# Performance work log

Hardware: AMD Instinct MI355X
Metric: run time of the kernel (lower is better)

Reference implementation:

```python
import jax, jax.numpy as jnp
import numpy as np

N = 50000   # nodes
E = 800000  # edges (avg degree 16)
D = 128     # hidden_channels
L = 4       # num_layers
ALPHA = 0.1


def setup_inputs() -> dict:
    key = jax.random.key(0)
    ks = jax.random.split(key, 6)
    x = jax.random.normal(ks[0], (N, D), dtype=jnp.float32)
    w = jax.random.uniform(ks[1], (E,), dtype=jnp.float32)
    src = jax.random.randint(ks[2], (E,), 0, N)
    dst = jax.random.randint(ks[3], (E,), 0, N)
    # stacked per-layer Linear params
    W = jax.random.normal(ks[4], (L, D, D), dtype=jnp.float32) / np.float32(np.sqrt(D))
    b = jax.random.normal(ks[5], (L, D), dtype=jnp.float32) * 0.01
    # GPR coefficients: alpha*(1-alpha)^k, last = (1-alpha)^L
    temp_np = ALPHA * (1 - ALPHA) ** np.arange(L + 1)
    temp_np[-1] = (1 - ALPHA) ** L
    temp = jnp.asarray(temp_np, dtype=jnp.float32)
    return {"x": x, "w": w, "src": src, "dst": dst, "W": W, "b": b, "temp": temp}


def reference(x, w, src, dst, W, b, temp):
    # eval mode: dropout / dropout_adj are no-ops; edge_attn=False
    hidden = x * temp[0]
    for i in range(L):
        h = x @ W[i] + b[i]                 # [N, D] linear
        msg = h[src] * w[:, None]           # gather + edge-weight, [E, D]
        x = jax.ops.segment_sum(msg, dst, num_segments=N)  # scatter-sum
        x = jax.nn.relu(x)
        hidden = hidden + x * temp[i + 1]
    return hidden
```

## Files before the change

kernel.cpp:

```cpp
#include <hip/hip_runtime.h>
#include <hip/hip_fp16.h>

#define N_NODES 50000
#define N_EDGES 800000
#define DIM 128
#define LAYERS 4
#define SLOT 48
#define EPB 8
#define CNT_STRIDE 6250

#define BUCKET_BLOCKS 3128
#define WT_BLOCKS 256
#define INIT_BLOCKS 3125

typedef __attribute__((ext_vector_type(8))) _Float16 half8;
typedef __attribute__((ext_vector_type(4))) float float4v;
typedef __attribute__((ext_vector_type(2))) float float2v;

__device__ __forceinline__ int pack_edge(int s, float w) {
    return (int)(((unsigned)__half_as_ushort(__float2half(w)) << 16) | (unsigned)(s & 0xFFFF));
}

__device__ __forceinline__ void fp8x8_to_f32(uint2 v, float* f) {
    float2v a = __builtin_amdgcn_cvt_pk_f32_fp8(v.x, false);
    float2v b = __builtin_amdgcn_cvt_pk_f32_fp8(v.x, true);
    float2v c = __builtin_amdgcn_cvt_pk_f32_fp8(v.y, false);
    float2v d = __builtin_amdgcn_cvt_pk_f32_fp8(v.y, true);
    f[0] = a[0]; f[1] = a[1]; f[2] = b[0]; f[3] = b[1];
    f[4] = c[0]; f[5] = c[1]; f[6] = d[0]; f[7] = d[1];
}

__device__ __forceinline__ uint2 f32x8_to_fp8(const float* f) {
    unsigned lo = 0, hi = 0;
    lo = __builtin_amdgcn_cvt_pk_fp8_f32(f[0], f[1], lo, false);
    lo = __builtin_amdgcn_cvt_pk_fp8_f32(f[2], f[3], lo, true);
    hi = __builtin_amdgcn_cvt_pk_fp8_f32(f[4], f[5], hi, false);
    hi = __builtin_amdgcn_cvt_pk_fp8_f32(f[6], f[7], hi, true);
    return make_uint2(lo, hi);
}

__device__ __forceinline__ void bucket_one(int d, int s, float wv, int g,
                                           int* __restrict__ cnt,
                                           int* __restrict__ edge_buf) {
    if ((d & 7) == g) {
        int pos = atomicAdd(&cnt[g * CNT_STRIDE + (d >> 3)], 1);
        edge_buf[(size_t)d * SLOT + pos] = pack_edge(s, wv);
    }
}

__global__ __launch_bounds__(256) void prep_kernel(const int* __restrict__ src,
                                                   const int* __restrict__ dst,
                                                   const float* __restrict__ w,
                                                   int* __restrict__ cnt,
                                                   int* __restrict__ edge_buf,
                                                   const float* __restrict__ W,
                                                   __half* __restrict__ Wt,
                                                   const float4* __restrict__ x,
                                                   uint2* __restrict__ xh0) {
    int bid = blockIdx.x;
    int tid = threadIdx.x;
    if (bid < BUCKET_BLOCKS) {
        int g     = bid & 7;
        int chunk = bid >> 3;
        int base  = (chunk * 256 + tid) * EPB;
        if (base >= N_EDGES) return;
        int4   d4a = *(const int4*)(dst + base);
        int4   d4b = *(const int4*)(dst + base + 4);
        int4   s4a = *(const int4*)(src + base);
        int4   s4b = *(const int4*)(src + base + 4);
        float4 w4a = *(const float4*)(w + base);
        float4 w4b = *(const float4*)(w + base + 4);
        bucket_one(d4a.x, s4a.x, w4a.x, g, cnt, edge_buf);
        bucket_one(d4a.y, s4a.y, w4a.y, g, cnt, edge_buf);
        bucket_one(d4a.z, s4a.z, w4a.z, g, cnt, edge_buf);
        bucket_one(d4a.w, s4a.w, w4a.w, g, cnt, edge_buf);
        bucket_one(d4b.x, s4b.x, w4b.x, g, cnt, edge_buf);
        bucket_one(d4b.y, s4b.y, w4b.y, g, cnt, edge_buf);
        bucket_one(d4b.z, s4b.z, w4b.z, g, cnt, edge_buf);
        bucket_one(d4b.w, s4b.w, w4b.w, g, cnt, edge_buf);
    } else if (bid < BUCKET_BLOCKS + WT_BLOCKS) {
        int i = (bid - BUCKET_BLOCKS) * 256 + tid;
        int l   = i >> 14;
        int rem = i & 16383;
        int k = rem >> 7;
        int n = rem & 127;
        Wt[(size_t)l * DIM * DIM + n * DIM + k] =
            __float2half(W[(size_t)l * DIM * DIM + k * DIM + n]);
    } else {
        int i = (bid - BUCKET_BLOCKS - WT_BLOCKS) * 256 + tid;
        float4 a = x[(size_t)i * 2];
        float4 b = x[(size_t)i * 2 + 1];
        float f[8] = { a.x, a.y, a.z, a.w, b.x, b.y, b.z, b.w };
        xh0[i] = f32x8_to_fp8(f);
    }
}

__device__ __forceinline__ void batch8(const uint2* __restrict__ x8,
                                       int m, int base, int cnt_r, int r, int c,
                                       float* accf, float& wsum) {
    uint2 v[8]; float wv[8];
    #pragma unroll
    for (int u = 0; u < 8; ++u) {
        int jj = base + u;
        int p  = __shfl(m, (r << 4) | (jj & 15), 64);
        bool live = (jj < cnt_r);
        wv[u] = live
                  ? __half2float(__ushort_as_half((unsigned short)((unsigned)p >> 16)))
                  : 0.f;
        uint2 vv = make_uint2(0u, 0u);
        if (live) vv = x8[(size_t)(p & 0xFFFF) * 16 + c];
        v[u] = vv;
    }
    #pragma unroll
    for (int u = 0; u < 8; ++u) {
        wsum += wv[u];
        float f[8];
        fp8x8_to_f32(v[u], f);
        #pragma unroll
        for (int t = 0; t < 8; ++t)
            accf[t] += wv[u] * f[t];
    }
}

#define AP 136
template <bool FINAL>
__global__ __launch_bounds__(256) void layer_kernel(const uint2* __restrict__ xin8,
                                                    const int* __restrict__ cnt_arr,
                                                    const int* __restrict__ edge_buf,
                                                    const __half* __restrict__ Wt,
                                                    const float* __restrict__ bl,
                                                    uint2* __restrict__ xout,
                                                    float* __restrict__ hidden,
                                                    const float* __restrict__ temp,
                                                    const uint2* __restrict__ x0h,
                                                    const uint2* __restrict__ x1h,
                                                    const uint2* __restrict__ x2h) {
    __shared__ __half Ah[16][AP];
    __shared__ float winS[16];
    int tid  = threadIdx.x;
    int wave = tid >> 6;
    int lane = tid & 63;
    int r = lane >> 4;
    int c = lane & 15;
    int node0  = blockIdx.x * 16 + wave * 4;
    int node_r = node0 + r;

    size_t mb = (size_t)node_r * SLOT;
    int m0 = edge_buf[mb + c];
    int m1 = edge_buf[mb + 16 + c];
    int cnt_r = cnt_arr[(node_r & 7) * CNT_STRIDE + (node_r >> 3)];

    int maxc = cnt_r;
    maxc = max(maxc, __shfl_xor(maxc, 16, 64));
    maxc = max(maxc, __shfl_xor(maxc, 32, 64));

    float accf[8];
    #pragma unroll
    for (int t = 0; t < 8; ++t) accf[t] = 0.f;
    float wsum = 0.f;

    batch8(xin8, m0, 0, cnt_r, r, c, accf, wsum);
    batch8(xin8, m0, 8, cnt_r, r, c, accf, wsum);
    if (maxc > 16) {
        batch8(xin8, m1, 16, cnt_r, r, c, accf, wsum);
        batch8(xin8, m1, 24, cnt_r, r, c, accf, wsum);
    }
    if (maxc > 32) {
        int m2 = edge_buf[mb + 32 + c];
        batch8(xin8, m2, 32, cnt_r, r, c, accf, wsum);
        batch8(xin8, m2, 40, cnt_r, r, c, accf, wsum);
    }

    union { __half2 hh[4]; float4 f4; } ua;
    ua.hh[0] = __floats2half2_rn(accf[0], accf[1]);
    ua.hh[1] = __floats2half2_rn(accf[2], accf[3]);
    ua.hh[2] = __floats2half2_rn(accf[4], accf[5]);
    ua.hh[3] = __floats2half2_rn(accf[6], accf[7]);
    int lr = wave * 4 + r;
    *(float4*)&Ah[lr][c * 8] = ua.f4;
    if (c == 0) winS[lr] = wsum;
    __syncthreads();

    int am  = lane & 15;
    int ak8 = (lane >> 4) * 8;
    float4v acc0 = (float4v)(0.f), acc1 = (float4v)(0.f);
    #pragma unroll
    for (int kk = 0; kk < 4; ++kk) {
        int k0 = kk * 32 + ak8;
        half8 a  = *(const half8*)&Ah[am][k0];
        half8 b0 = *(const half8*)(Wt + (size_t)(wave * 32 + am) * DIM + k0);
        half8 b1 = *(const half8*)(Wt + (size_t)(wave * 32 + 16 + am) * DIM + k0);
        acc0 = __builtin_amdgcn_mfma_f32_16x16x32_f16(a, b0, acc0, 0, 0, 0);
        acc1 = __builtin_amdgcn_mfma_f32_16x16x32_f16(a, b1, acc1, 0, 0, 0);
    }
    __syncthreads();

    int q  = lane >> 4;
    int cc = lane & 15;
    {
        int col = wave * 32 + cc;
        float bv = bl[col];
        #pragma unroll
        for (int j = 0; j < 4; ++j) {
            int row = q * 4 + j;
            Ah[row][col] = __float2half(fmaxf(acc0[j] + winS[row] * bv, 0.f));
        }
        col = wave * 32 + 16 + cc;
        bv = bl[col];
        #pragma unroll
        for (int j = 0; j < 4; ++j) {
            int row = q * 4 + j;
            Ah[row][col] = __float2half(fmaxf(acc1[j] + winS[row] * bv, 0.f));
        }
    }
    __syncthreads();

    int row = tid >> 4;
    int ch  = tid & 15;
    int gnode = blockIdx.x * 16 + row;
    half8 hv = *(const half8*)&Ah[row][ch * 8];
    size_t ro = (size_t)gnode * 16 + ch;

    if constexpr (!FINAL) {
        float f[8];
        #pragma unroll
        for (int t = 0; t < 8; ++t) f[t] = (float)hv[t];
        xout[ro] = f32x8_to_fp8(f);
    } else {
        float t0 = temp[0], t1 = temp[1], t2 = temp[2], t3 = temp[3], t4 = temp[4];
        uint2 u0 = x0h[ro], u1 = x1h[ro], u2 = x2h[ro], u3 = xin8[ro];
        float f0[8], f1[8], f2[8], f3[8];
        fp8x8_to_f32(u0, f0);
        fp8x8_to_f32(u1, f1);
        fp8x8_to_f32(u2, f2);
        fp8x8_to_f32(u3, f3);
        float out[8];
        #pragma unroll
        for (int t = 0; t < 8; ++t)
            out[t] = t0 * f0[t] + t1 * f1[t] + t2 * f2[t]
                   + t3 * f3[t] + t4 * (float)hv[t];
        size_t o = (size_t)gnode * DIM + ch * 8;
        *(float4*)(hidden + o)     = make_float4(out[0], out[1], out[2], out[3]);
        *(float4*)(hidden + o + 4) = make_float4(out[4], out[5], out[6], out[7]);
    }
}

extern "C" void kernel_launch(void* const* d_in, const int* in_sizes, int n_in,
                              void* d_out, int out_size, void* d_ws, size_t ws_size,
                              hipStream_t stream) {
    const float* x    = (const float*)d_in[0];
    const float* w    = (const float*)d_in[1];
    const int*   src  = (const int*)d_in[2];
    const int*   dst  = (const int*)d_in[3];
    const float* W    = (const float*)d_in[4];
    const float* b    = (const float*)d_in[5];
    const float* temp = (const float*)d_in[6];
    float* hidden = (float*)d_out;

    char* ws = (char*)d_ws;
    uint2* X0 = (uint2*)ws;                  ws += (size_t)N_NODES * DIM;
    uint2* X1 = (uint2*)ws;                  ws += (size_t)N_NODES * DIM;
    uint2* X2 = (uint2*)ws;                  ws += (size_t)N_NODES * DIM;
    uint2* X3 = (uint2*)ws;                  ws += (size_t)N_NODES * DIM;
    __half* Wt = (__half*)ws;                ws += (size_t)LAYERS * DIM * DIM * sizeof(__half);
    int* cnt = (int*)ws;                     ws += (size_t)N_NODES * sizeof(int);
    int* edge_buf = (int*)ws;                ws += (size_t)(N_NODES * SLOT + 64) * sizeof(int);

    hipMemsetAsync(cnt, 0, (size_t)N_NODES * sizeof(int), stream);
    prep_kernel<<<BUCKET_BLOCKS + WT_BLOCKS + INIT_BLOCKS, 256, 0, stream>>>(
        src, dst, w, cnt, edge_buf, W, Wt, (const float4*)x, X0);

    const int layer_blocks = N_NODES / 16;
    layer_kernel<false><<<layer_blocks, 256, 0, stream>>>(
        X0, cnt, edge_buf, Wt + 0 * DIM * DIM, b + 0 * DIM,
        X1, hidden, temp, nullptr, nullptr, nullptr);
    layer_kernel<false><<<layer_blocks, 256, 0, stream>>>(
        X1, cnt, edge_buf, Wt + 1 * DIM * DIM, b + 1 * DIM,
        X2, hidden, temp, nullptr, nullptr, nullptr);
    layer_kernel<false><<<layer_blocks, 256, 0, stream>>>(
        X2, cnt, edge_buf, Wt + 2 * DIM * DIM, b + 2 * DIM,
        X3, hidden, temp, nullptr, nullptr, nullptr);
    layer_kernel<true><<<layer_blocks, 256, 0, stream>>>(
        X3, cnt, edge_buf, Wt + 3 * DIM * DIM, b + 3 * DIM,
        nullptr, hidden, temp, X0, X1, X2);
}
```

Baseline: 244.6 us.

## Process 32 nodes per block with 16-byte gathers and 8 lanes per node

Each layer block now handles 32 nodes instead of 16. Each node is served by 8 lanes that each gather 16 fp8 features (uint4) per edge, so every lane issues half as many wider loads. Each wave now computes a 16x64 tile of the 32x128 MFMA product, so each weight fragment is reused across more rows. The cost is twice the accumulator registers per lane, possible lower occupancy, and a bounds check for the last partial block.

```diff
diff --git a/kernel.cpp b/kernel.cpp
--- a/kernel.cpp
+++ b/kernel.cpp
@@ -12,6 +12,7 @@
 #define BUCKET_BLOCKS 3128
 #define WT_BLOCKS 256
 #define INIT_BLOCKS 3125
+#define LAYER_BLOCKS 1563
 
 typedef __attribute__((ext_vector_type(8))) _Float16 half8;
 typedef __attribute__((ext_vector_type(4))) float float4v;
@@ -95,36 +96,36 @@
     }
 }
 
-__device__ __forceinline__ void batch8(const uint2* __restrict__ x8,
-                                       int m, int base, int cnt_r, int r, int c,
-                                       float* accf, float& wsum) {
-    uint2 v[8]; float wv[8];
+__device__ __forceinline__ void batch8w(const uint4* __restrict__ x16,
+                                        int m, int base, int cnt_r, int sgb, int c2,
+                                        float* accf, float& wsum) {
+    uint4 v[8]; float wv[8];
     #pragma unroll
     for (int u = 0; u < 8; ++u) {
-        int jj = base + u;
-        int p  = __shfl(m, (r << 4) | (jj & 15), 64);
-        bool live = (jj < cnt_r);
+        int p = __shfl(m, sgb | u, 64);
+        bool live = (base + u) < cnt_r;
         wv[u] = live
                   ? __half2float(__ushort_as_half((unsigned short)((unsigned)p >> 16)))
                   : 0.f;
-        uint2 vv = make_uint2(0u, 0u);
-        if (live) vv = x8[(size_t)(p & 0xFFFF) * 16 + c];
+        uint4 vv = make_uint4(0u, 0u, 0u, 0u);
+        if (live) vv = x16[(size_t)(p & 0xFFFF) * 8 + c2];
         v[u] = vv;
     }
     #pragma unroll
     for (int u = 0; u < 8; ++u) {
         wsum += wv[u];
-        float f[8];
-        fp8x8_to_f32(v[u], f);
-        #pragma unroll
-        for (int t = 0; t < 8; ++t)
+        float f[16];
+        fp8x8_to_f32(make_uint2(v[u].x, v[u].y), f);
+        fp8x8_to_f32(make_uint2(v[u].z, v[u].w), f + 8);
+        #pragma unroll
+        for (int t = 0; t < 16; ++t)
             accf[t] += wv[u] * f[t];
     }
 }
 
 #define AP 136
 template <bool FINAL>
-__global__ __launch_bounds__(256) void layer_kernel(const uint2* __restrict__ xin8,
+__global__ __launch_bounds__(256) void layer_kernel(const uint4* __restrict__ xin16,
                                                     const int* __restrict__ cnt_arr,
                                                     const int* __restrict__ edge_buf,
                                                     const __half* __restrict__ Wt,
@@ -135,113 +136,126 @@
                                                     const uint2* __restrict__ x0h,
                                                     const uint2* __restrict__ x1h,
                                                     const uint2* __restrict__ x2h) {
-    __shared__ __half Ah[16][AP];
-    __shared__ float winS[16];
+    __shared__ __half Ah[32][AP];
+    __shared__ float winS[32];
     int tid  = threadIdx.x;
     int wave = tid >> 6;
     int lane = tid & 63;
-    int r = lane >> 4;
-    int c = lane & 15;
-    int node0  = blockIdx.x * 16 + wave * 4;
-    int node_r = node0 + r;
-
-    size_t mb = (size_t)node_r * SLOT;
-    int m0 = edge_buf[mb + c];
-    int m1 = edge_buf[mb + 16 + c];
-    int cnt_r = cnt_arr[(node_r & 7) * CNT_STRIDE + (node_r >> 3)];
+    int sg  = lane >> 3;
+    int c2  = lane & 7;
+    int sgb = lane & 0x38;
+    int node_r = blockIdx.x * 32 + wave * 8 + sg;
+    bool valid = node_r < N_NODES;
+    int nidx = valid ? node_r : 0;
+
+    size_t mb = (size_t)nidx * SLOT;
+    int m0 = edge_buf[mb + c2];
+    int m1 = edge_buf[mb + 8 + c2];
+    int m2 = edge_buf[mb + 16 + c2];
+    int m3 = edge_buf[mb + 24 + c2];
+    int cnt_r = valid ? cnt_arr[(nidx & 7) * CNT_STRIDE + (nidx >> 3)] : 0;
 
     int maxc = cnt_r;
+    maxc = max(maxc, __shfl_xor(maxc, 8, 64));
     maxc = max(maxc, __shfl_xor(maxc, 16, 64));
     maxc = max(maxc, __shfl_xor(maxc, 32, 64));
 
-    float accf[8];
-    #pragma unroll
-    for (int t = 0; t < 8; ++t) accf[t] = 0.f;
+    float accf[16];
+    #pragma unroll
+    for (int t = 0; t < 16; ++t) accf[t] = 0.f;
     float wsum = 0.f;
 
-    batch8(xin8, m0, 0, cnt_r, r, c, accf, wsum);
-    batch8(xin8, m0, 8, cnt_r, r, c, accf, wsum);
+    batch8w(xin16, m0, 0, cnt_r, sgb, c2, accf, wsum);
+    batch8w(xin16, m1, 8, cnt_r, sgb, c2, accf, wsum);
     if (maxc > 16) {
-        batch8(xin8, m1, 16, cnt_r, r, c, accf, wsum);
-        batch8(xin8, m1, 24, cnt_r, r, c, accf, wsum);
+        batch8w(xin16, m2, 16, cnt_r, sgb, c2, accf, wsum);
+        batch8w(xin16, m3, 24, cnt_r, sgb, c2, accf, wsum);
     }
     if (maxc > 32) {
-        int m2 = edge_buf[mb + 32 + c];
-        batch8(xin8, m2, 32, cnt_r, r, c, accf, wsum);
-        batch8(xin8, m2, 40, cnt_r, r, c, accf, wsum);
-    }
-
-    union { __half2 hh[4]; float4 f4; } ua;
-    ua.hh[0] = __floats2half2_rn(accf[0], accf[1]);
-    ua.hh[1] = __floats2half2_rn(accf[2], accf[3]);
-    ua.hh[2] = __floats2half2_rn(accf[4], accf[5]);
-    ua.hh[3] = __floats2half2_rn(accf[6], accf[7]);
-    int lr = wave * 4 + r;
-    *(float4*)&Ah[lr][c * 8] = ua.f4;
-    if (c == 0) winS[lr] = wsum;
+        int m4 = edge_buf[mb + 32 + c2];
+        int m5 = edge_buf[mb + 40 + c2];
+        batch8w(xin16, m4, 32, cnt_r, sgb, c2, accf, wsum);
+        batch8w(xin16, m5, 40, cnt_r, sgb, c2, accf, wsum);
+    }
+
+    {
+        union { __half2 hh[8]; float4 f4[2]; } ua;
+        #pragma unroll
+        for (int t = 0; t < 8; ++t)
+            ua.hh[t] = __floats2half2_rn(accf[2 * t], accf[2 * t + 1]);
+        int lr = wave * 8 + sg;
+        *(float4*)&Ah[lr][c2 * 16]     = ua.f4[0];
+        *(float4*)&Ah[lr][c2 * 16 + 8] = ua.f4[1];
+        if (c2 == 0) winS[lr] = wsum;
+    }
     __syncthreads();
 
     int am  = lane & 15;
     int ak8 = (lane >> 4) * 8;
-    float4v acc0 = (float4v)(0.f), acc1 = (float4v)(0.f);
+    int rt  = (wave & 1) * 16;
+    int ct  = (wave >> 1) * 64;
+    float4v acc[4];
+    #pragma unroll
+    for (int j = 0; j < 4; ++j) acc[j] = (float4v)(0.f);
     #pragma unroll
     for (int kk = 0; kk < 4; ++kk) {
         int k0 = kk * 32 + ak8;
-        half8 a  = *(const half8*)&Ah[am][k0];
-        half8 b0 = *(const half8*)(Wt + (size_t)(wave * 32 + am) * DIM + k0);
-        half8 b1 = *(const half8*)(Wt + (size_t)(wave * 32 + 16 + am) * DIM + k0);
-        acc0 = __builtin_amdgcn_mfma_f32_16x16x32_f16(a, b0, acc0, 0, 0, 0);
-        acc1 = __builtin_amdgcn_mfma_f32_16x16x32_f16(a, b1, acc1, 0, 0, 0);
+        half8 a = *(const half8*)&Ah[rt + am][k0];
+        #pragma unroll
+        for (int j = 0; j < 4; ++j) {
+            half8 bj = *(const half8*)(Wt + (size_t)(ct + j * 16 + am) * DIM + k0);
+            acc[j] = __builtin_amdgcn_mfma_f32_16x16x32_f16(a, bj, acc[j], 0, 0, 0);
+        }
     }
     __syncthreads();
 
-    int q  = lane >> 4;
-    int cc = lane & 15;
     {
-        int col = wave * 32 + cc;
-        float bv = bl[col];
+        int q  = lane >> 4;
+        int cc = lane & 15;
         #pragma unroll
         for (int j = 0; j < 4; ++j) {
-            int row = q * 4 + j;
-            Ah[row][col] = __float2half(fmaxf(acc0[j] + winS[row] * bv, 0.f));
+            int col = ct + j * 16 + cc;
+            float bv = bl[col];
+            #pragma unroll
+            for (int jj = 0; jj < 4; ++jj) {
+                int row = rt + q * 4 + jj;
+                Ah[row][col] = __float2half(fmaxf(acc[j][jj] + winS[row] * bv, 0.f));
+            }
         }
-        col = wave * 32 + 16 + cc;
-        bv = bl[col];
-        #pragma unroll
-        for (int j = 0; j < 4; ++j) {
-            int row = q * 4 + j;
-            Ah[row][col] = __float2half(fmaxf(acc1[j] + winS[row] * bv, 0.f));
+    }
+    __syncthreads();
+
+    #pragma unroll
+    for (int h = 0; h < 2; ++h) {
+        int row = h * 16 + (tid >> 4);
+        int ch  = tid & 15;
+        int gnode = blockIdx.x * 32 + row;
+        if (gnode >= N_NODES) continue;
+        half8 hv = *(const half8*)&Ah[row][ch * 8];
+        size_t ro = (size_t)gnode * 16 + ch;
+        if constexpr (!FINAL) {
+            float f[8];
+            #pragma unroll
+            for (int t = 0; t < 8; ++t) f[t] = (float)hv[t];
+            xout[ro] = f32x8_to_fp8(f);
+        } else {
+            float t0 = temp[0], t1 = temp[1], t2 = temp[2], t3 = temp[3], t4 = temp[4];
+            uint2 u0 = x0h[ro], u1 = x1h[ro], u2 = x2h[ro];
+            uint2 u3 = ((const uint2*)xin16)[ro];
+            float f0[8], f1[8], f2[8], f3[8];
+            fp8x8_to_f32(u0, f0);
+            fp8x8_to_f32(u1, f1);
+            fp8x8_to_f32(u2, f2);
+            fp8x8_to_f32(u3, f3);
+            float out[8];
+            #pragma unroll
+            for (int t = 0; t < 8; ++t)
+                out[t] = t0 * f0[t] + t1 * f1[t] + t2 * f2[t]
+                       + t3 * f3[t] + t4 * (float)hv[t];
+            size_t o = (size_t)gnode * DIM + ch * 8;
+            *(float4*)(hidden + o)     = make_float4(out[0], out[1], out[2], out[3]);
+            *(float4*)(hidden + o + 4) = make_float4(out[4], out[5], out[6], out[7]);
         }
-    }
-    __syncthreads();
-
-    int row = tid >> 4;
-    int ch  = tid & 15;
-    int gnode = blockIdx.x * 16 + row;
-    half8 hv = *(const half8*)&Ah[row][ch * 8];
-    size_t ro = (size_t)gnode * 16 + ch;
-
-    if constexpr (!FINAL) {
-        float f[8];
-        #pragma unroll
-        for (int t = 0; t < 8; ++t) f[t] = (float)hv[t];
-        xout[ro] = f32x8_to_fp8(f);
-    } else {
-        float t0 = temp[0], t1 = temp[1], t2 = temp[2], t3 = temp[3], t4 = temp[4];
-        uint2 u0 = x0h[ro], u1 = x1h[ro], u2 = x2h[ro], u3 = xin8[ro];
-        float f0[8], f1[8], f2[8], f3[8];
-        fp8x8_to_f32(u0, f0);
-        fp8x8_to_f32(u1, f1);
-        fp8x8_to_f32(u2, f2);
-        fp8x8_to_f32(u3, f3);
-        float out[8];
-        #pragma unroll
-        for (int t = 0; t < 8; ++t)
-            out[t] = t0 * f0[t] + t1 * f1[t] + t2 * f2[t]
-                   + t3 * f3[t] + t4 * (float)hv[t];
-        size_t o = (size_t)gnode * DIM + ch * 8;
-        *(float4*)(hidden + o)     = make_float4(out[0], out[1], out[2], out[3]);
-        *(float4*)(hidden + o + 4) = make_float4(out[4], out[5], out[6], out[7]);
     }
 }
 
@@ -270,17 +284,16 @@
     prep_kernel<<<BUCKET_BLOCKS + WT_BLOCKS + INIT_BLOCKS, 256, 0, stream>>>(
         src, dst, w, cnt, edge_buf, W, Wt, (const float4*)x, X0);
 
-    const int layer_blocks = N_NODES / 16;
-    layer_kernel<false><<<layer_blocks, 256, 0, stream>>>(
-        X0, cnt, edge_buf, Wt + 0 * DIM * DIM, b + 0 * DIM,
+    layer_kernel<false><<<LAYER_BLOCKS, 256, 0, stream>>>(
+        (const uint4*)X0, cnt, edge_buf, Wt + 0 * DIM * DIM, b + 0 * DIM,
         X1, hidden, temp, nullptr, nullptr, nullptr);
-    layer_kernel<false><<<layer_blocks, 256, 0, stream>>>(
-        X1, cnt, edge_buf, Wt + 1 * DIM * DIM, b + 1 * DIM,
+    layer_kernel<false><<<LAYER_BLOCKS, 256, 0, stream>>>(
+        (const uint4*)X1, cnt, edge_buf, Wt + 1 * DIM * DIM, b + 1 * DIM,
         X2, hidden, temp, nullptr, nullptr, nullptr);
-    layer_kernel<false><<<layer_blocks, 256, 0, stream>>>(
-        X2, cnt, edge_buf, Wt + 2 * DIM * DIM, b + 2 * DIM,
+    layer_kernel<false><<<LAYER_BLOCKS, 256, 0, stream>>>(
+        (const uint4*)X2, cnt, edge_buf, Wt + 2 * DIM * DIM, b + 2 * DIM,
         X3, hidden, temp, nullptr, nullptr, nullptr);
-    layer_kernel<true><<<layer_blocks, 256, 0, stream>>>(
-        X3, cnt, edge_buf, Wt + 3 * DIM * DIM, b + 3 * DIM,
+    layer_kernel<true><<<LAYER_BLOCKS, 256, 0, stream>>>(
+        (const uint4*)X3, cnt, edge_buf, Wt + 3 * DIM * DIM, b + 3 * DIM,
         nullptr, hidden, temp, X0, X1, X2);
 }
```

New measurement: 265.1 us. +8.4%, slower.
